# Kernel optimization log

Measured on AMD Instinct MI355X. Metric: run time of the kernel, lower is better.

The kernel has to match this reference:

```python
import jax, jax.numpy as jnp
import numpy as np

N = 65536   # num rois (batch*num_rois)
C = 512     # input_channels
D = 512     # output_dims = num_heads * head_dims
H = 8       # num_heads
HD = 64     # head_dims
L = 16      # hardcoded expand size in forward
BN_EPS = 1e-5


def _bn(x, gamma, beta, mean, var):
    # eval-mode BatchNorm1d over channel axis 1 of [N, D, L]
    inv = gamma / jnp.sqrt(var + BN_EPS)
    return x * inv[None, :, None] + (beta - mean * inv)[None, :, None]


def setup_inputs() -> dict:
    key = jax.random.key(0)
    ks = jax.random.split(key, 12)
    w = lambda k, shape: jax.random.normal(k, shape, jnp.float32) * 0.05
    return {
        "features": jax.random.normal(ks[0], (N, C), jnp.float32),
        "features2": jax.random.normal(ks[1], (N, C), jnp.float32),
        "Wk": w(ks[2], (D, C)),      # key_proj conv1d weight (shared for pos & key)
        "Wv1": w(ks[3], (D, C)),     # value_proj conv1d #1
        "Wv2": w(ks[4], (D, D)),     # value_proj conv1d #2
        "bn1_gamma": jnp.ones((D,), jnp.float32),
        "bn1_beta": jnp.zeros((D,), jnp.float32),
        "bn1_mean": jax.random.normal(ks[5], (D,), jnp.float32) * 0.1,
        "bn1_var": jax.random.uniform(ks[6], (D,), jnp.float32, 0.5, 1.5),
        "bn2_gamma": jnp.ones((D,), jnp.float32),
        "bn2_beta": jnp.zeros((D,), jnp.float32),
        "bn2_mean": jax.random.normal(ks[7], (D,), jnp.float32) * 0.1,
        "bn2_var": jax.random.uniform(ks[8], (D,), jnp.float32, 0.5, 1.5),
        "Wa": w(ks[9], (H, D)),      # attention_proj conv1d
        "Wqk": w(ks[10], (D, D)),    # qk_coef Linear
        "Wvc": w(ks[11], (D, D)),    # v_coef Linear
    }


def reference(features, features2, Wk, Wv1, Wv2,
              bn1_gamma, bn1_beta, bn1_mean, bn1_var,
              bn2_gamma, bn2_beta, bn2_mean, bn2_var,
              Wa, Wqk, Wvc):
    # expand [N, C] -> [N, C, L] (all L columns identical, as in torch .expand)
    f = jnp.broadcast_to(features[:, :, None], (features.shape[0], features.shape[1], L))
    f2 = jnp.broadcast_to(features2[:, :, None], (features2.shape[0], features2.shape[1], L))

    # key_proj (shared weights) on both inputs: 1x1 conv + ReLU
    pos = jax.nn.relu(jnp.einsum('oc,ncl->nol', Wk, f))
    key_e = jax.nn.relu(jnp.einsum('oc,ncl->nol', Wk, f2))

    # value_proj: conv -> BN -> ReLU -> conv -> BN -> ReLU
    h = jax.nn.relu(_bn(jnp.einsum('oc,ncl->nol', Wv1, f2), bn1_gamma, bn1_beta, bn1_mean, bn1_var))
    value = jax.nn.relu(_bn(jnp.einsum('od,ndl->nol', Wv2, h), bn2_gamma, bn2_beta, bn2_mean, bn2_var))

    pk = pos * key_e                                    # [N, D, L]
    v_coef = jax.nn.sigmoid(pos.mean(axis=2) @ Wvc.T)   # [N, D]
    qk_coef = jax.nn.sigmoid(pk.mean(axis=2) @ Wqk.T)   # [N, D]

    value = value + pos * v_coef[:, :, None]
    attn_emb = pk * qk_coef[:, :, None]

    attn = jnp.einsum('hd,ndl->nhl', Wa, attn_emb)      # [N, H, L]
    attn = jax.nn.softmax(attn, axis=-1)
    attn = jnp.repeat(attn, HD, axis=1)                 # [N, H*HD, L], head-major

    return jnp.sum(attn * value, axis=-1)               # [N, D]
```

## Files before the change

kernel.cpp:

```cpp
#include <hip/hip_runtime.h>
#include <hip/hip_bf16.h>
#include <cstdint>
#include <cstddef>


#define DIM 512
#define NROWS 65536
#define MBLK 64

typedef __bf16 bf16;
typedef __attribute__((ext_vector_type(8))) __bf16 bf16x8;
typedef __attribute__((ext_vector_type(4))) __bf16 bf16x4;
typedef __attribute__((ext_vector_type(4))) float f32x4;

__device__ __forceinline__ float sigmoidf_(float x) {
  return 1.0f / (1.0f + __expf(-x));
}

__device__ __forceinline__ int lds_off(int row, int cb) {
  return row * (DIM * 2) + (cb ^ ((row & 15) << 4));
}

__global__ __launch_bounds__(256) void cvt_f32_bf16(
    const float* __restrict__ s, bf16* __restrict__ d, int n4) {
  int i = blockIdx.x * 256 + threadIdx.x;
  if (i < n4) {
    f32x4 v = ((const f32x4*)s)[i];
    bf16x4 o;
    o[0] = (bf16)v[0]; o[1] = (bf16)v[1]; o[2] = (bf16)v[2]; o[3] = (bf16)v[3];
    ((bf16x4*)d)[i] = o;
  }
}

__device__ __forceinline__ void stage_panel(char* As, const float* __restrict__ g,
                                            int t) {
#pragma unroll
  for (int it = 0; it < 8; ++it) {
    int c = it * 512 + t;
    f32x4 v0 = *(const f32x4*)(g + (size_t)c * 8);
    f32x4 v1 = *(const f32x4*)(g + (size_t)c * 8 + 4);
    bf16x8 o;
    o[0] = (bf16)v0[0]; o[1] = (bf16)v0[1]; o[2] = (bf16)v0[2]; o[3] = (bf16)v0[3];
    o[4] = (bf16)v1[0]; o[5] = (bf16)v1[1]; o[6] = (bf16)v1[2]; o[7] = (bf16)v1[3];
    *(bf16x8*)(As + lds_off(c >> 6, (c & 63) * 16)) = o;
  }
}

__device__ __forceinline__ void gemm_core(f32x4 (&acc)[4][4], const char* As,
                                          const bf16* __restrict__ W, int lr,
                                          int kq, int wn) {
  const bf16* bp = W + (size_t)(wn + lr) * DIM + kq * 8;
  bf16x8 bq0[4], bq1[4], bq2[4];
#pragma unroll
  for (int j = 0; j < 4; j++) bq0[j] = *(const bf16x8*)(bp + j * 16 * DIM);
#pragma unroll
  for (int j = 0; j < 4; j++) bq1[j] = *(const bf16x8*)(bp + j * 16 * DIM + 32);
#pragma unroll
  for (int j = 0; j < 4; j++) bq2[j] = bq1[j];
  for (int kb = 0; kb < DIM; kb += 32) {
    bf16x8 a[4];
#pragma unroll
    for (int i = 0; i < 4; i++)
      a[i] = *(const bf16x8*)(As + (i * 16 + lr) * (DIM * 2) +
                              ((kb * 2 + kq * 16) ^ (lr << 4)));
    if (kb + 64 < DIM) {
#pragma unroll
      for (int j = 0; j < 4; j++)
        bq2[j] = *(const bf16x8*)(bp + j * 16 * DIM + kb + 64);
    }
#pragma unroll
    for (int i = 0; i < 4; i++)
#pragma unroll
      for (int j = 0; j < 4; j++)
        acc[i][j] = __builtin_amdgcn_mfma_f32_16x16x32_bf16(a[i], bq0[j],
                                                            acc[i][j], 0, 0, 0);
#pragma unroll
    for (int j = 0; j < 4; j++) {
      bq0[j] = bq1[j];
      bq1[j] = bq2[j];
    }
  }
}

__global__ __launch_bounds__(512, 2) void fusedA(
    const float* __restrict__ f, const bf16* __restrict__ Wk,
    const bf16* __restrict__ Wvc, bf16x4* __restrict__ pvws) {
  __shared__ __align__(16) char As[MBLK * DIM * 2];
  const int t = threadIdx.x;
  const int lane = t & 63;
  const int lr = lane & 15;
  const int kq = lane >> 4;
  const int wn = (t >> 6) * 64;
  const size_t m0 = (size_t)blockIdx.x * MBLK;

  stage_panel(As, f + m0 * DIM, t);
  __syncthreads();

  f32x4 acc[4][4];
#pragma unroll
  for (int i = 0; i < 4; i++)
#pragma unroll
    for (int j = 0; j < 4; j++) acc[i][j] = (f32x4){0.f, 0.f, 0.f, 0.f};
  gemm_core(acc, As, Wk, lr, kq, wn);

  __syncthreads();
#pragma unroll
  for (int i = 0; i < 4; i++)
#pragma unroll
    for (int j = 0; j < 4; j++)
#pragma unroll
      for (int r = 0; r < 4; r++) {
        int m = i * 16 + kq * 4 + r;
        int n = wn + j * 16 + lr;
        *(bf16*)(As + lds_off(m, n * 2)) = (bf16)fmaxf(acc[i][j][r], 0.f);
      }
  __syncthreads();

#pragma unroll
  for (int i = 0; i < 4; i++)
#pragma unroll
    for (int j = 0; j < 4; j++) acc[i][j] = (f32x4){0.f, 0.f, 0.f, 0.f};
  gemm_core(acc, As, Wvc, lr, kq, wn);

#pragma unroll
  for (int i = 0; i < 4; i++)
#pragma unroll
    for (int j = 0; j < 4; j++) {
      bf16x4 o;
#pragma unroll
      for (int r = 0; r < 4; r++) {
        int m = i * 16 + kq * 4 + r;
        int n = wn + j * 16 + lr;
        float p = (float)(*(const bf16*)(As + lds_off(m, n * 2)));
        o[r] = (bf16)(sigmoidf_(acc[i][j][r]) * p);
      }
      pvws[((size_t)blockIdx.x * 16 + i * 4 + j) * 512 + t] = o;
    }
}

__global__ __launch_bounds__(512, 2) void fusedB(
    const float* __restrict__ f2, const bf16* __restrict__ Wv1,
    const bf16* __restrict__ Wv2, const bf16x4* __restrict__ pvws,
    float* __restrict__ out, const float* __restrict__ bg1,
    const float* __restrict__ bb1, const float* __restrict__ bm1,
    const float* __restrict__ bv1, const float* __restrict__ bg2,
    const float* __restrict__ bb2, const float* __restrict__ bm2,
    const float* __restrict__ bv2) {
  __shared__ __align__(16) char As[MBLK * DIM * 2];
  const int t = threadIdx.x;
  const int lane = t & 63;
  const int lr = lane & 15;
  const int kq = lane >> 4;
  const int wn = (t >> 6) * 64;
  const size_t m0 = (size_t)blockIdx.x * MBLK;

  stage_panel(As, f2 + m0 * DIM, t);
  __syncthreads();

  f32x4 acc[4][4];
#pragma unroll
  for (int i = 0; i < 4; i++)
#pragma unroll
    for (int j = 0; j < 4; j++) acc[i][j] = (f32x4){0.f, 0.f, 0.f, 0.f};
  gemm_core(acc, As, Wv1, lr, kq, wn);

  float iv1[4], bc1[4];
#pragma unroll
  for (int j = 0; j < 4; j++) {
    int c = wn + j * 16 + lr;
    float s = bg1[c] * rsqrtf(bv1[c] + 1e-5f);
    iv1[j] = s;
    bc1[j] = bb1[c] - bm1[c] * s;
  }

  __syncthreads();
#pragma unroll
  for (int i = 0; i < 4; i++)
#pragma unroll
    for (int j = 0; j < 4; j++)
#pragma unroll
      for (int r = 0; r < 4; r++) {
        int m = i * 16 + kq * 4 + r;
        int n = wn + j * 16 + lr;
        float v = fmaxf(acc[i][j][r] * iv1[j] + bc1[j], 0.f);
        *(bf16*)(As + lds_off(m, n * 2)) = (bf16)v;
      }
  __syncthreads();

#pragma unroll
  for (int i = 0; i < 4; i++)
#pragma unroll
    for (int j = 0; j < 4; j++) acc[i][j] = (f32x4){0.f, 0.f, 0.f, 0.f};
  gemm_core(acc, As, Wv2, lr, kq, wn);

  float iv2[4], bc2[4];
#pragma unroll
  for (int j = 0; j < 4; j++) {
    int c = wn + j * 16 + lr;
    float s = bg2[c] * rsqrtf(bv2[c] + 1e-5f);
    iv2[j] = s;
    bc2[j] = bb2[c] - bm2[c] * s;
  }

#pragma unroll
  for (int i = 0; i < 4; i++)
#pragma unroll
    for (int j = 0; j < 4; j++) {
      bf16x4 pv = pvws[((size_t)blockIdx.x * 16 + i * 4 + j) * 512 + t];
#pragma unroll
      for (int r = 0; r < 4; r++) {
        int m = i * 16 + kq * 4 + r;
        int n = wn + j * 16 + lr;
        float v = fmaxf(acc[i][j][r] * iv2[j] + bc2[j], 0.f) + (float)pv[r];
        out[(m0 + m) * DIM + n] = v;
      }
    }
}

extern "C" void kernel_launch(void* const* d_in, const int* in_sizes, int n_in,
                              void* d_out, int out_size, void* d_ws,
                              size_t ws_size, hipStream_t stream) {
  const float* features  = (const float*)d_in[0];
  const float* features2 = (const float*)d_in[1];
  const float* Wk  = (const float*)d_in[2];
  const float* Wv1 = (const float*)d_in[3];
  const float* Wv2 = (const float*)d_in[4];
  const float* g1 = (const float*)d_in[5];
  const float* b1 = (const float*)d_in[6];
  const float* m1 = (const float*)d_in[7];
  const float* v1 = (const float*)d_in[8];
  const float* g2 = (const float*)d_in[9];
  const float* b2 = (const float*)d_in[10];
  const float* m2 = (const float*)d_in[11];
  const float* v2 = (const float*)d_in[12];
  const float* Wvc = (const float*)d_in[15];
  float* out = (float*)d_out;

  bf16* wkb  = (bf16*)d_ws;
  bf16* wv1b = wkb + (size_t)DIM * DIM;
  bf16* wv2b = wv1b + (size_t)DIM * DIM;
  bf16* wvcb = wv2b + (size_t)DIM * DIM;
  bf16* pvws = wvcb + (size_t)DIM * DIM;

  {
    int n4 = DIM * DIM / 4;
    dim3 cg(n4 / 256), cb(256);
    cvt_f32_bf16<<<cg, cb, 0, stream>>>(Wk, wkb, n4);
    cvt_f32_bf16<<<cg, cb, 0, stream>>>(Wvc, wvcb, n4);
    cvt_f32_bf16<<<cg, cb, 0, stream>>>(Wv1, wv1b, n4);
    cvt_f32_bf16<<<cg, cb, 0, stream>>>(Wv2, wv2b, n4);
  }

  dim3 grid(NROWS / MBLK);
  dim3 block(512);
  fusedA<<<grid, block, 0, stream>>>(features, wkb, wvcb, (bf16x4*)pvws);
  fusedB<<<grid, block, 0, stream>>>(features2, wv1b, wv2b,
                                     (const bf16x4*)pvws, out,
                                     g1, b1, m1, v1, g2, b2, m2, v2);
}
```

Before: 626.5 us.

## Fuse the two row-panel kernels into one and double-buffer A fragments

```diff
diff --git a/kernel.cpp b/kernel.cpp
--- a/kernel.cpp
+++ b/kernel.cpp
@@ -19,6 +19,12 @@
 
 __device__ __forceinline__ int lds_off(int row, int cb) {
   return row * (DIM * 2) + (cb ^ ((row & 15) << 4));
+}
+
+__device__ __forceinline__ bf16x8 lda(const char* As, int i, int lr, int kq,
+                                      int kb) {
+  return *(const bf16x8*)(As + (i * 16 + lr) * (DIM * 2) +
+                          ((kb * 2 + kq * 16) ^ (lr << 4)));
 }
 
 __global__ __launch_bounds__(256) void cvt_f32_bf16(
@@ -32,17 +38,24 @@
   }
 }
 
-__device__ __forceinline__ void stage_panel(char* As, const float* __restrict__ g,
-                                            int t) {
+__device__ __forceinline__ void stage2(char* PA, const float* __restrict__ ga,
+                                       char* PB, const float* __restrict__ gb,
+                                       int t) {
 #pragma unroll
   for (int it = 0; it < 8; ++it) {
     int c = it * 512 + t;
-    f32x4 v0 = *(const f32x4*)(g + (size_t)c * 8);
-    f32x4 v1 = *(const f32x4*)(g + (size_t)c * 8 + 4);
-    bf16x8 o;
-    o[0] = (bf16)v0[0]; o[1] = (bf16)v0[1]; o[2] = (bf16)v0[2]; o[3] = (bf16)v0[3];
-    o[4] = (bf16)v1[0]; o[5] = (bf16)v1[1]; o[6] = (bf16)v1[2]; o[7] = (bf16)v1[3];
-    *(bf16x8*)(As + lds_off(c >> 6, (c & 63) * 16)) = o;
+    f32x4 a0 = *(const f32x4*)(ga + (size_t)c * 8);
+    f32x4 a1 = *(const f32x4*)(ga + (size_t)c * 8 + 4);
+    f32x4 b0 = *(const f32x4*)(gb + (size_t)c * 8);
+    f32x4 b1 = *(const f32x4*)(gb + (size_t)c * 8 + 4);
+    bf16x8 oa, ob;
+    oa[0] = (bf16)a0[0]; oa[1] = (bf16)a0[1]; oa[2] = (bf16)a0[2]; oa[3] = (bf16)a0[3];
+    oa[4] = (bf16)a1[0]; oa[5] = (bf16)a1[1]; oa[6] = (bf16)a1[2]; oa[7] = (bf16)a1[3];
+    ob[0] = (bf16)b0[0]; ob[1] = (bf16)b0[1]; ob[2] = (bf16)b0[2]; ob[3] = (bf16)b0[3];
+    ob[4] = (bf16)b1[0]; ob[5] = (bf16)b1[1]; ob[6] = (bf16)b1[2]; ob[7] = (bf16)b1[3];
+    int off = lds_off(c >> 6, (c & 63) * 16);
+    *(bf16x8*)(PA + off) = oa;
+    *(bf16x8*)(PB + off) = ob;
   }
 }
 
@@ -50,42 +63,63 @@
                                           const bf16* __restrict__ W, int lr,
                                           int kq, int wn) {
   const bf16* bp = W + (size_t)(wn + lr) * DIM + kq * 8;
-  bf16x8 bq0[4], bq1[4], bq2[4];
-#pragma unroll
-  for (int j = 0; j < 4; j++) bq0[j] = *(const bf16x8*)(bp + j * 16 * DIM);
-#pragma unroll
-  for (int j = 0; j < 4; j++) bq1[j] = *(const bf16x8*)(bp + j * 16 * DIM + 32);
-#pragma unroll
-  for (int j = 0; j < 4; j++) bq2[j] = bq1[j];
-  for (int kb = 0; kb < DIM; kb += 32) {
-    bf16x8 a[4];
+  bf16x8 a0[4], a1[4], b0[4], b1[4];
+#pragma unroll
+  for (int j = 0; j < 4; j++) b0[j] = *(const bf16x8*)(bp + j * 16 * DIM);
+#pragma unroll
+  for (int j = 0; j < 4; j++) b1[j] = *(const bf16x8*)(bp + j * 16 * DIM + 32);
+#pragma unroll
+  for (int i = 0; i < 4; i++) a0[i] = lda(As, i, lr, kq, 0);
+#pragma unroll
+  for (int kb = 0; kb < DIM; kb += 64) {
+#pragma unroll
+    for (int i = 0; i < 4; i++) a1[i] = lda(As, i, lr, kq, kb + 32);
 #pragma unroll
     for (int i = 0; i < 4; i++)
-      a[i] = *(const bf16x8*)(As + (i * 16 + lr) * (DIM * 2) +
-                              ((kb * 2 + kq * 16) ^ (lr << 4)));
+#pragma unroll
+      for (int j = 0; j < 4; j++)
+        acc[i][j] = __builtin_amdgcn_mfma_f32_16x16x32_bf16(a0[i], b0[j],
+                                                            acc[i][j], 0, 0, 0);
     if (kb + 64 < DIM) {
 #pragma unroll
       for (int j = 0; j < 4; j++)
-        bq2[j] = *(const bf16x8*)(bp + j * 16 * DIM + kb + 64);
+        b0[j] = *(const bf16x8*)(bp + j * 16 * DIM + kb + 64);
+#pragma unroll
+      for (int i = 0; i < 4; i++) a0[i] = lda(As, i, lr, kq, kb + 64);
     }
 #pragma unroll
     for (int i = 0; i < 4; i++)
 #pragma unroll
       for (int j = 0; j < 4; j++)
-        acc[i][j] = __builtin_amdgcn_mfma_f32_16x16x32_bf16(a[i], bq0[j],
+        acc[i][j] = __builtin_amdgcn_mfma_f32_16x16x32_bf16(a1[i], b1[j],
                                                             acc[i][j], 0, 0, 0);
-#pragma unroll
-    for (int j = 0; j < 4; j++) {
-      bq0[j] = bq1[j];
-      bq1[j] = bq2[j];
+    if (kb + 96 < DIM) {
+#pragma unroll
+      for (int j = 0; j < 4; j++)
+        b1[j] = *(const bf16x8*)(bp + j * 16 * DIM + kb + 96);
     }
   }
 }
 
-__global__ __launch_bounds__(512, 2) void fusedA(
-    const float* __restrict__ f, const bf16* __restrict__ Wk,
-    const bf16* __restrict__ Wvc, bf16x4* __restrict__ pvws) {
-  __shared__ __align__(16) char As[MBLK * DIM * 2];
+__device__ __forceinline__ void zero_acc(f32x4 (&acc)[4][4]) {
+#pragma unroll
+  for (int i = 0; i < 4; i++)
+#pragma unroll
+    for (int j = 0; j < 4; j++) acc[i][j] = (f32x4){0.f, 0.f, 0.f, 0.f};
+}
+
+__global__ __launch_bounds__(512, 2) void fused_all(
+    const float* __restrict__ f, const float* __restrict__ f2,
+    const bf16* __restrict__ Wk, const bf16* __restrict__ Wvc,
+    const bf16* __restrict__ Wv1, const bf16* __restrict__ Wv2,
+    float* __restrict__ out, const float* __restrict__ bg1,
+    const float* __restrict__ bb1, const float* __restrict__ bm1,
+    const float* __restrict__ bv1, const float* __restrict__ bg2,
+    const float* __restrict__ bb2, const float* __restrict__ bm2,
+    const float* __restrict__ bv2) {
+  __shared__ __align__(16) char P1[MBLK * DIM * 2];
+  __shared__ __align__(16) char P2[MBLK * DIM * 2];
+
   const int t = threadIdx.x;
   const int lane = t & 63;
   const int lr = lane & 15;
@@ -93,77 +127,43 @@
   const int wn = (t >> 6) * 64;
   const size_t m0 = (size_t)blockIdx.x * MBLK;
 
-  stage_panel(As, f + m0 * DIM, t);
+  stage2(P1, f + m0 * DIM, P2, f2 + m0 * DIM, t);
   __syncthreads();
 
   f32x4 acc[4][4];
-#pragma unroll
-  for (int i = 0; i < 4; i++)
-#pragma unroll
-    for (int j = 0; j < 4; j++) acc[i][j] = (f32x4){0.f, 0.f, 0.f, 0.f};
-  gemm_core(acc, As, Wk, lr, kq, wn);
-
-  __syncthreads();
-#pragma unroll
-  for (int i = 0; i < 4; i++)
-#pragma unroll
-    for (int j = 0; j < 4; j++)
-#pragma unroll
-      for (int r = 0; r < 4; r++) {
-        int m = i * 16 + kq * 4 + r;
-        int n = wn + j * 16 + lr;
-        *(bf16*)(As + lds_off(m, n * 2)) = (bf16)fmaxf(acc[i][j][r], 0.f);
-      }
-  __syncthreads();
-
-#pragma unroll
-  for (int i = 0; i < 4; i++)
-#pragma unroll
-    for (int j = 0; j < 4; j++) acc[i][j] = (f32x4){0.f, 0.f, 0.f, 0.f};
-  gemm_core(acc, As, Wvc, lr, kq, wn);
-
-#pragma unroll
-  for (int i = 0; i < 4; i++)
-#pragma unroll
-    for (int j = 0; j < 4; j++) {
-      bf16x4 o;
-#pragma unroll
-      for (int r = 0; r < 4; r++) {
-        int m = i * 16 + kq * 4 + r;
-        int n = wn + j * 16 + lr;
-        float p = (float)(*(const bf16*)(As + lds_off(m, n * 2)));
-        o[r] = (bf16)(sigmoidf_(acc[i][j][r]) * p);
-      }
-      pvws[((size_t)blockIdx.x * 16 + i * 4 + j) * 512 + t] = o;
-    }
-}
-
-__global__ __launch_bounds__(512, 2) void fusedB(
-    const float* __restrict__ f2, const bf16* __restrict__ Wv1,
-    const bf16* __restrict__ Wv2, const bf16x4* __restrict__ pvws,
-    float* __restrict__ out, const float* __restrict__ bg1,
-    const float* __restrict__ bb1, const float* __restrict__ bm1,
-    const float* __restrict__ bv1, const float* __restrict__ bg2,
-    const float* __restrict__ bb2, const float* __restrict__ bm2,
-    const float* __restrict__ bv2) {
-  __shared__ __align__(16) char As[MBLK * DIM * 2];
-  const int t = threadIdx.x;
-  const int lane = t & 63;
-  const int lr = lane & 15;
-  const int kq = lane >> 4;
-  const int wn = (t >> 6) * 64;
-  const size_t m0 = (size_t)blockIdx.x * MBLK;
-
-  stage_panel(As, f2 + m0 * DIM, t);
-  __syncthreads();
-
-  f32x4 acc[4][4];
-#pragma unroll
-  for (int i = 0; i < 4; i++)
-#pragma unroll
-    for (int j = 0; j < 4; j++) acc[i][j] = (f32x4){0.f, 0.f, 0.f, 0.f};
-  gemm_core(acc, As, Wv1, lr, kq, wn);
-
+
+  zero_acc(acc);
+  gemm_core(acc, P1, Wk, lr, kq, wn);
+  __syncthreads();
+#pragma unroll
+  for (int i = 0; i < 4; i++)
+#pragma unroll
+    for (int j = 0; j < 4; j++)
+#pragma unroll
+      for (int r = 0; r < 4; r++) {
+        int m = i * 16 + kq * 4 + r;
+        int n = wn + j * 16 + lr;
+        *(bf16*)(P1 + lds_off(m, n * 2)) = (bf16)fmaxf(acc[i][j][r], 0.f);
+      }
+  __syncthreads();
+
+  zero_acc(acc);
+  gemm_core(acc, P1, Wvc, lr, kq, wn);
+  bf16x4 pvr[4][4];
+#pragma unroll
+  for (int i = 0; i < 4; i++)
+#pragma unroll
+    for (int j = 0; j < 4; j++)
+#pragma unroll
+      for (int r = 0; r < 4; r++) {
+        int m = i * 16 + kq * 4 + r;
+        int n = wn + j * 16 + lr;
+        float p = (float)(*(const bf16*)(P1 + lds_off(m, n * 2)));
+        pvr[i][j][r] = (bf16)(sigmoidf_(acc[i][j][r]) * p);
+      }
+
+  zero_acc(acc);
+  gemm_core(acc, P2, Wv1, lr, kq, wn);
   float iv1[4], bc1[4];
 #pragma unroll
   for (int j = 0; j < 4; j++) {
@@ -172,7 +172,6 @@
     iv1[j] = s;
     bc1[j] = bb1[c] - bm1[c] * s;
   }
-
   __syncthreads();
 #pragma unroll
   for (int i = 0; i < 4; i++)
@@ -183,16 +182,12 @@
         int m = i * 16 + kq * 4 + r;
         int n = wn + j * 16 + lr;
         float v = fmaxf(acc[i][j][r] * iv1[j] + bc1[j], 0.f);
-        *(bf16*)(As + lds_off(m, n * 2)) = (bf16)v;
-      }
-  __syncthreads();
-
-#pragma unroll
-  for (int i = 0; i < 4; i++)
-#pragma unroll
-    for (int j = 0; j < 4; j++) acc[i][j] = (f32x4){0.f, 0.f, 0.f, 0.f};
-  gemm_core(acc, As, Wv2, lr, kq, wn);
-
+        *(bf16*)(P2 + lds_off(m, n * 2)) = (bf16)v;
+      }
+  __syncthreads();
+
+  zero_acc(acc);
+  gemm_core(acc, P2, Wv2, lr, kq, wn);
   float iv2[4], bc2[4];
 #pragma unroll
   for (int j = 0; j < 4; j++) {
@@ -201,20 +196,17 @@
     iv2[j] = s;
     bc2[j] = bb2[c] - bm2[c] * s;
   }
-
-#pragma unroll
-  for (int i = 0; i < 4; i++)
-#pragma unroll
-    for (int j = 0; j < 4; j++) {
-      bf16x4 pv = pvws[((size_t)blockIdx.x * 16 + i * 4 + j) * 512 + t];
-#pragma unroll
-      for (int r = 0; r < 4; r++) {
-        int m = i * 16 + kq * 4 + r;
-        int n = wn + j * 16 + lr;
-        float v = fmaxf(acc[i][j][r] * iv2[j] + bc2[j], 0.f) + (float)pv[r];
+#pragma unroll
+  for (int i = 0; i < 4; i++)
+#pragma unroll
+    for (int j = 0; j < 4; j++)
+#pragma unroll
+      for (int r = 0; r < 4; r++) {
+        int m = i * 16 + kq * 4 + r;
+        int n = wn + j * 16 + lr;
+        float v = fmaxf(acc[i][j][r] * iv2[j] + bc2[j], 0.f) + (float)pvr[i][j][r];
         out[(m0 + m) * DIM + n] = v;
       }
-    }
 }
 
 extern "C" void kernel_launch(void* const* d_in, const int* in_sizes, int n_in,
@@ -237,10 +229,9 @@
   float* out = (float*)d_out;
 
   bf16* wkb  = (bf16*)d_ws;
-  bf16* wv1b = wkb + (size_t)DIM * DIM;
+  bf16* wvcb = wkb + (size_t)DIM * DIM;
+  bf16* wv1b = wvcb + (size_t)DIM * DIM;
   bf16* wv2b = wv1b + (size_t)DIM * DIM;
-  bf16* wvcb = wv2b + (size_t)DIM * DIM;
-  bf16* pvws = wvcb + (size_t)DIM * DIM;
 
   {
     int n4 = DIM * DIM / 4;
@@ -253,8 +244,7 @@
 
   dim3 grid(NROWS / MBLK);
   dim3 block(512);
-  fusedA<<<grid, block, 0, stream>>>(features, wkb, wvcb, (bf16x4*)pvws);
-  fusedB<<<grid, block, 0, stream>>>(features2, wv1b, wv2b,
-                                     (const bf16x4*)pvws, out,
-                                     g1, b1, m1, v1, g2, b2, m2, v2);
-}
+  fused_all<<<grid, block, 0, stream>>>(features, features2, wkb, wvcb, wv1b,
+                                        wv2b, out, g1, b1, m1, v1, g2, b2, m2,
+                                        v2);
+}
```

Measured after the change: 667.2 us. 6.5% more time.
